# Kernel tuning notes

Measured on AMD Instinct MI355X. Metric: run time of the kernel, lower is better.

## Reference

```python
import jax, jax.numpy as jnp
import numpy as np

HDIM = 32
U_DIM = 8
HID = 128
T = 65536
DYN_GAIN = 0.02
STATE_DAMP = 0.1
H_CLIP = 5.0
DT = np.float32(5.0 / 60.0)  # 5 minutes in hours


def _xavier(key, shape):
    fan_in, fan_out = shape[0], shape[1]
    limit = np.sqrt(6.0 / (fan_in + fan_out)).astype(np.float32)
    return jax.random.uniform(key, shape, jnp.float32, -limit, limit)


def setup_inputs() -> dict:
    key = jax.random.key(0)
    ks = jax.random.split(key, 8)
    U = jax.random.normal(ks[0], (T, U_DIM), jnp.float32)
    params = {
        "U": U,
        "h0": jnp.zeros((1, HDIM), jnp.float32),
        "W1": _xavier(ks[1], (HDIM + U_DIM, HID)), "b1": jnp.zeros((HID,), jnp.float32),
        "W2": _xavier(ks[2], (HID, HID)), "b2": jnp.zeros((HID,), jnp.float32),
        "W3": _xavier(ks[3], (HID, HDIM)), "b3": jnp.zeros((HDIM,), jnp.float32),
        "Wd": _xavier(ks[4], (HDIM, 1)), "bd": jnp.zeros((1,), jnp.float32),
        "Wt": _xavier(ks[5], (HDIM, 1)), "bt": jnp.zeros((1,), jnp.float32),
        "Wc": _xavier(ks[6], (HDIM, 1)), "bc": jnp.zeros((1,), jnp.float32),
    }
    return params


def reference(U, h0, W1, b1, W2, b2, W3, b3, Wd, bd, Wt, bt, Wc, bc):
    dt = jnp.float32(DT)

    def dyn(h, u):
        # h: [1, HDIM], u: [1, U_DIM]
        x = jnp.concatenate([h, u], axis=-1)
        z = jax.nn.silu(x @ W1 + b1)
        z = jax.nn.silu(z @ W2 + b2)
        drift = z @ W3 + b3
        return DYN_GAIN * drift - STATE_DAMP * h

    def step(h, u_t):
        u = u_t[None, :]  # [1, U_DIM]
        # readout of current state (before the RK4 step, as in the torch loop)
        d = (h @ Wd + bd)[..., 0]  # [1]
        t = (h @ Wt + bt)[..., 0]
        c = (h @ Wc + bc)[..., 0]
        k1 = dyn(h, u)
        k2 = dyn(h + 0.5 * dt * k1, u)
        k3 = dyn(h + 0.5 * dt * k2, u)
        k4 = dyn(h + dt * k3, u)
        h_next = h + dt / 6.0 * (k1 + 2.0 * k2 + 2.0 * k3 + k4)
        h_next = jnp.nan_to_num(h_next, nan=0.0, posinf=0.0, neginf=0.0)
        h_next = jnp.clip(jnp.tanh(h_next), -H_CLIP, H_CLIP)
        return h_next, (d, t, c)

    h_last, (ds, ts, cs) = jax.lax.scan(step, h0, U)
    # ds/ts/cs: [T, 1] -> [T]
    return ds.squeeze(-1), ts.squeeze(-1), cs.squeeze(-1), h_last
```

## Files before the change

kernel.cpp:

```cpp
#include <hip/hip_runtime.h>
#include <math.h>


constexpr int T_STEPS = 65536;
constexpr int HD  = 32;
constexpr int HID = 128;

typedef float v2f __attribute__((ext_vector_type(2)));

__device__ __forceinline__ v2f fma2(v2f a, v2f b, v2f c) {
    return __builtin_elementwise_fma(a, b, c);
}

__device__ __forceinline__ float silu_f(float a) {
    return a / (1.0f + __expf(-a));
}

__device__ __forceinline__ void wg_barrier() {
    asm volatile("s_waitcnt lgkmcnt(0)" ::: "memory");
    __builtin_amdgcn_s_barrier();
    asm volatile("" ::: "memory");
}

__global__ __launch_bounds__(128, 1)
void node_scan(const float* __restrict__ U,
               const float* __restrict__ h0,
               const float* __restrict__ W1, const float* __restrict__ b1,
               const float* __restrict__ W2, const float* __restrict__ b2,
               const float* __restrict__ W3, const float* __restrict__ b3,
               const float* __restrict__ Wd, const float* __restrict__ bd,
               const float* __restrict__ Wt, const float* __restrict__ bt,
               const float* __restrict__ Wc, const float* __restrict__ bc,
               float* __restrict__ out)
{
    const int tid = threadIdx.x;
    const int j   = tid;
    const int m   = tid & 31;
    const int seg = tid >> 5;
    const int wv  = tid >> 6;

    __shared__ __align__(16) float xbuf[HD];
    __shared__ __align__(16) float z1buf[HID];
    __shared__ __align__(16) float z2buf[HID];
    __shared__ __align__(16) float pb2[64];

    v2f w1p[20];
#pragma unroll
    for (int i = 0; i < 20; ++i) {
        w1p[i].x = W1[(2 * i) * HID + j];
        w1p[i].y = W1[(2 * i + 1) * HID + j];
    }
    const float b1r = b1[j];

    v2f w2p[64];
#pragma unroll
    for (int i = 0; i < 64; ++i) {
        w2p[i].x = W2[(2 * i) * HID + j];
        w2p[i].y = W2[(2 * i + 1) * HID + j];
    }
    const float b2r = b2[j];

    v2f w3p[16];
#pragma unroll
    for (int i = 0; i < 16; ++i) {
        w3p[i].x = W3[(seg * 32 + 2 * i) * HD + m];
        w3p[i].y = W3[(seg * 32 + 2 * i + 1) * HD + m];
    }
    const float b3r = b3[m];

    const float whr = (wv == 0) ? Wd[m] : Wt[m];
    const float wcr = Wc[m];
    const float bd0 = bd[0], bt0 = bt[0], bc0 = bc[0];

    float hm   = h0[m];
    float xm   = hm;
    float kacc = 0.0f;

    const float DT  = 5.0f / 60.0f;
    const float HDT = 0.5f * DT;
    const float W6  = DT / 6.0f;

    float4 ua = *(const float4*)(U);
    float4 ub = *(const float4*)(U + 4);

    xbuf[m] = xm;
    wg_barrier();

    for (int t = 0; t < T_STEPS; ++t) {
        const int tn = (t + 1 < T_STEPS) ? (t + 1) : t;
        const float4 na = *(const float4*)(U + tn * 8);
        const float4 nb = *(const float4*)(U + tn * 8 + 4);

        {
            float p  = hm * whr;
            float pc = hm * wcr;
            p += __shfl_xor(p, 16);  pc += __shfl_xor(pc, 16);
            p += __shfl_xor(p, 8);   pc += __shfl_xor(pc, 8);
            p += __shfl_xor(p, 4);   pc += __shfl_xor(pc, 4);
            p += __shfl_xor(p, 2);   pc += __shfl_xor(pc, 2);
            p += __shfl_xor(p, 1);   pc += __shfl_xor(pc, 1);
            if (tid == 0)  { out[t] = p + bd0; out[2 * T_STEPS + t] = pc + bc0; }
            if (tid == 64) { out[T_STEPS + t] = p + bt0; }
        }

        float upj;
        {
            v2f u0; u0.x = ua.x; u0.y = ua.y;
            v2f u1; u1.x = ua.z; u1.y = ua.w;
            v2f u2; u2.x = ub.x; u2.y = ub.y;
            v2f u3; u3.x = ub.z; u3.y = ub.w;
            v2f up = {b1r, 0.0f};
            up = fma2(u0, w1p[16], up);
            up = fma2(u1, w1p[17], up);
            up = fma2(u2, w1p[18], up);
            up = fma2(u3, w1p[19], up);
            upj = up.x + up.y;
        }

#pragma unroll
        for (int st = 0; st < 4; ++st) {
            v2f a0 = {upj, 0.0f}, a1 = {0.0f, 0.0f};
            const float4* xv = (const float4*)xbuf;
#pragma unroll
            for (int i4 = 0; i4 < 8; ++i4) {
                const float4 v = xv[i4];
                v2f lo; lo.x = v.x; lo.y = v.y;
                v2f hi; hi.x = v.z; hi.y = v.w;
                a0 = fma2(lo, w1p[2 * i4],     a0);
                a1 = fma2(hi, w1p[2 * i4 + 1], a1);
            }
            const v2f as = a0 + a1;
            z1buf[j] = silu_f(as.x + as.y);
            wg_barrier();

            v2f c0 = {b2r, 0.0f}, c1 = {0.0f, 0.0f};
            v2f c2 = {0.0f, 0.0f}, c3 = {0.0f, 0.0f};
            const float4* z1v = (const float4*)z1buf;
#pragma unroll
            for (int i4 = 0; i4 < 32; ++i4) {
                const float4 v = z1v[i4];
                v2f lo; lo.x = v.x; lo.y = v.y;
                v2f hi; hi.x = v.z; hi.y = v.w;
                if (i4 & 1) {
                    c2 = fma2(lo, w2p[2 * i4],     c2);
                    c3 = fma2(hi, w2p[2 * i4 + 1], c3);
                } else {
                    c0 = fma2(lo, w2p[2 * i4],     c0);
                    c1 = fma2(hi, w2p[2 * i4 + 1], c1);
                }
            }
            const v2f cs = (c0 + c1) + (c2 + c3);
            z2buf[j] = silu_f(cs.x + cs.y);
            __builtin_amdgcn_wave_barrier();

            v2f p0 = {0.0f, 0.0f}, p1 = {0.0f, 0.0f};
            const float4* z2v = (const float4*)(z2buf + seg * 32);
#pragma unroll
            for (int i4 = 0; i4 < 8; ++i4) {
                const float4 v = z2v[i4];
                v2f lo; lo.x = v.x; lo.y = v.y;
                v2f hi; hi.x = v.z; hi.y = v.w;
                p0 = fma2(lo, w3p[2 * i4],     p0);
                p1 = fma2(hi, w3p[2 * i4 + 1], p1);
            }
            const v2f ps = p0 + p1;
            float pr = ps.x + ps.y;
            pr += __shfl_xor(pr, 32);
            pb2[wv * 32 + m] = pr;
            wg_barrier();

            {
                const float drift = (pb2[m] + pb2[m + 32]) + b3r;
                const float k = 0.02f * drift - 0.1f * xm;
                if (st == 0)      { kacc = k;           xm = hm + HDT * k; }
                else if (st == 1) { kacc += 2.0f * k;   xm = hm + HDT * k; }
                else if (st == 2) { kacc += 2.0f * k;   xm = hm + DT  * k; }
                else {
                    kacc += k;
                    float hn = hm + W6 * kacc;
                    if (!isfinite(hn)) hn = 0.0f;
                    hn = tanhf(hn);
                    hn = fminf(fmaxf(hn, -5.0f), 5.0f);
                    hm = hn; xm = hn;
                }
                xbuf[m] = xm;
            }
            __builtin_amdgcn_wave_barrier();
        }
        ua = na; ub = nb;
    }

    if (tid < HD) out[3 * T_STEPS + tid] = hm;
}

extern "C" void kernel_launch(void* const* d_in, const int* in_sizes, int n_in,
                              void* d_out, int out_size, void* d_ws, size_t ws_size,
                              hipStream_t stream) {
    const float* U  = (const float*)d_in[0];
    const float* h0 = (const float*)d_in[1];
    const float* W1 = (const float*)d_in[2];
    const float* b1 = (const float*)d_in[3];
    const float* W2 = (const float*)d_in[4];
    const float* b2 = (const float*)d_in[5];
    const float* W3 = (const float*)d_in[6];
    const float* b3 = (const float*)d_in[7];
    const float* Wd = (const float*)d_in[8];
    const float* bd = (const float*)d_in[9];
    const float* Wt = (const float*)d_in[10];
    const float* bt = (const float*)d_in[11];
    const float* Wc = (const float*)d_in[12];
    const float* bc = (const float*)d_in[13];
    float* out = (float*)d_out;

    node_scan<<<1, 128, 0, stream>>>(U, h0, W1, b1, W2, b2, W3, b3,
                                     Wd, bd, Wt, bt, Wc, bc, out);
}
```

Before: 237.5 ms.

## Split layer-2 matvec by input half per wave and exchange partial sums

Each wave now computes partial layer-2 sums for all 128 outputs over only its own 64 z1 inputs. That lets the barrier after the z1 write become a wave-local barrier. Partial sums are then exchanged through shared memory behind one workgroup barrier, and both waves redundantly compute the full z2 vector. W3 and the pb2 layouts are re-indexed to match the new z2 ordering. The aim is to shorten the cross-wave wait on the serial per-step critical path, at the cost of extra LDS traffic and duplicated silu work.

```diff
diff --git a/kernel.cpp b/kernel.cpp
--- a/kernel.cpp
+++ b/kernel.cpp
@@ -35,13 +35,15 @@
 {
     const int tid = threadIdx.x;
     const int j   = tid;
+    const int l   = tid & 63;
     const int m   = tid & 31;
     const int seg = tid >> 5;
     const int wv  = tid >> 6;
 
     __shared__ __align__(16) float xbuf[HD];
     __shared__ __align__(16) float z1buf[HID];
-    __shared__ __align__(16) float z2buf[HID];
+    __shared__ __align__(16) float z2slot[HID];
+    __shared__ __align__(16) float pex[2 * HID];
     __shared__ __align__(16) float pb2[64];
 
     v2f w1p[20];
@@ -52,19 +54,22 @@
     }
     const float b1r = b1[j];
 
-    v2f w2p[64];
-#pragma unroll
-    for (int i = 0; i < 64; ++i) {
-        w2p[i].x = W2[(2 * i) * HID + j];
-        w2p[i].y = W2[(2 * i + 1) * HID + j];
-    }
-    const float b2r = b2[j];
+    v2f w2a[32], w2b[32];
+#pragma unroll
+    for (int kp = 0; kp < 32; ++kp) {
+        const int k = wv * 64 + 2 * kp;
+        w2a[kp].x = W2[k * HID + l];
+        w2a[kp].y = W2[(k + 1) * HID + l];
+        w2b[kp].x = W2[k * HID + l + 64];
+        w2b[kp].y = W2[(k + 1) * HID + l + 64];
+    }
+    const float b2a = b2[l], b2b = b2[l + 64];
 
     v2f w3p[16];
 #pragma unroll
     for (int i = 0; i < 16; ++i) {
-        w3p[i].x = W3[(seg * 32 + 2 * i) * HD + m];
-        w3p[i].y = W3[(seg * 32 + 2 * i + 1) * HD + m];
+        w3p[i].x = W3[(seg * 16 + i) * HD + m];
+        w3p[i].y = W3[(seg * 16 + i + 64) * HD + m];
     }
     const float b3r = b3[m];
 
@@ -131,30 +136,38 @@
             }
             const v2f as = a0 + a1;
             z1buf[j] = silu_f(as.x + as.y);
-            wg_barrier();
-
-            v2f c0 = {b2r, 0.0f}, c1 = {0.0f, 0.0f};
-            v2f c2 = {0.0f, 0.0f}, c3 = {0.0f, 0.0f};
-            const float4* z1v = (const float4*)z1buf;
-#pragma unroll
-            for (int i4 = 0; i4 < 32; ++i4) {
+            __builtin_amdgcn_wave_barrier();
+
+            v2f aA0 = {0.0f, 0.0f}, aA1 = {0.0f, 0.0f};
+            v2f aB0 = {0.0f, 0.0f}, aB1 = {0.0f, 0.0f};
+            const float4* z1v = (const float4*)(z1buf + wv * 64);
+#pragma unroll
+            for (int i4 = 0; i4 < 16; ++i4) {
                 const float4 v = z1v[i4];
                 v2f lo; lo.x = v.x; lo.y = v.y;
                 v2f hi; hi.x = v.z; hi.y = v.w;
-                if (i4 & 1) {
-                    c2 = fma2(lo, w2p[2 * i4],     c2);
-                    c3 = fma2(hi, w2p[2 * i4 + 1], c3);
-                } else {
-                    c0 = fma2(lo, w2p[2 * i4],     c0);
-                    c1 = fma2(hi, w2p[2 * i4 + 1], c1);
-                }
-            }
-            const v2f cs = (c0 + c1) + (c2 + c3);
-            z2buf[j] = silu_f(cs.x + cs.y);
+                aA0 = fma2(lo, w2a[2 * i4],     aA0);
+                aA1 = fma2(hi, w2a[2 * i4 + 1], aA1);
+                aB0 = fma2(lo, w2b[2 * i4],     aB0);
+                aB1 = fma2(hi, w2b[2 * i4 + 1], aB1);
+            }
+            const v2f sA = aA0 + aA1;
+            const v2f sB = aB0 + aB1;
+            float2 mine;
+            mine.x = sA.x + sA.y;
+            mine.y = sB.x + sB.y;
+            ((float2*)pex)[wv * 64 + l] = mine;
+            wg_barrier();
+
+            const float2 po = ((const float2*)pex)[(1 ^ wv) * 64 + l];
+            const float z2A = silu_f(mine.x + po.x + b2a);
+            const float z2B = silu_f(mine.y + po.y + b2b);
+            float2 zs; zs.x = z2A; zs.y = z2B;
+            ((float2*)z2slot)[l] = zs;
             __builtin_amdgcn_wave_barrier();
 
             v2f p0 = {0.0f, 0.0f}, p1 = {0.0f, 0.0f};
-            const float4* z2v = (const float4*)(z2buf + seg * 32);
+            const float4* z2v = (const float4*)(z2slot + seg * 32);
 #pragma unroll
             for (int i4 = 0; i4 < 8; ++i4) {
                 const float4 v = z2v[i4];
@@ -166,11 +179,12 @@
             const v2f ps = p0 + p1;
             float pr = ps.x + ps.y;
             pr += __shfl_xor(pr, 32);
-            pb2[wv * 32 + m] = pr;
+            pb2[2 * m + wv] = pr;
             wg_barrier();
 
             {
-                const float drift = (pb2[m] + pb2[m + 32]) + b3r;
+                const float2 pp = ((const float2*)pb2)[m];
+                const float drift = (pp.x + pp.y) + b3r;
                 const float k = 0.02f * drift - 0.1f * xm;
                 if (st == 0)      { kacc = k;           xm = hm + HDT * k; }
                 else if (st == 1) { kacc += 2.0f * k;   xm = hm + HDT * k; }
```

Result: no change. 235.9 ms (-0.7%).

## Split second MLP layer's reduction across four waves with partial-sum exchange

Applied to the files above, without the earlier changes.

The block grows from 128 to 256 threads. Layer 2's K dimension is split between wave pairs, so each thread runs half as many serial FMAs and holds half as many W2 registers. The two partial sums are combined through shared memory behind one workgroup barrier. Layer 1 is now computed redundantly by both wave pairs so each wave can read its own z1 slice after only a wave barrier, and the readouts are spread so each wave handles one output. The goal is a shorter per-step critical path in this latency-bound serial scan, at the cost of more waves taking part in barriers and some duplicated layer-1 work.

```diff
diff --git a/kernel.cpp b/kernel.cpp
--- a/kernel.cpp
+++ b/kernel.cpp
@@ -22,7 +22,7 @@
     asm volatile("" ::: "memory");
 }
 
-__global__ __launch_bounds__(128, 1)
+__global__ __launch_bounds__(256, 1)
 void node_scan(const float* __restrict__ U,
                const float* __restrict__ h0,
                const float* __restrict__ W1, const float* __restrict__ b1,
@@ -34,43 +34,49 @@
                float* __restrict__ out)
 {
     const int tid = threadIdx.x;
-    const int j   = tid;
+    const int lam = tid & 63;
+    const int w   = tid >> 6;
+    const int wk  = w & 1;
+    const int wo  = w >> 1;
+    const int j1  = lam + wk * 64;
+    const int o   = lam + wo * 64;
     const int m   = tid & 31;
-    const int seg = tid >> 5;
-    const int wv  = tid >> 6;
+    const int sub = (tid >> 5) & 1;
 
     __shared__ __align__(16) float xbuf[HD];
     __shared__ __align__(16) float z1buf[HID];
     __shared__ __align__(16) float z2buf[HID];
-    __shared__ __align__(16) float pb2[64];
+    __shared__ __align__(16) float pex[2 * HID];
+    __shared__ __align__(16) float pdrift[64];
 
     v2f w1p[20];
 #pragma unroll
     for (int i = 0; i < 20; ++i) {
-        w1p[i].x = W1[(2 * i) * HID + j];
-        w1p[i].y = W1[(2 * i + 1) * HID + j];
-    }
-    const float b1r = b1[j];
-
-    v2f w2p[64];
-#pragma unroll
-    for (int i = 0; i < 64; ++i) {
-        w2p[i].x = W2[(2 * i) * HID + j];
-        w2p[i].y = W2[(2 * i + 1) * HID + j];
-    }
-    const float b2r = b2[j];
+        w1p[i].x = W1[(2 * i) * HID + j1];
+        w1p[i].y = W1[(2 * i + 1) * HID + j1];
+    }
+    const float b1r = b1[j1];
+
+    v2f w2p[32];
+#pragma unroll
+    for (int kp = 0; kp < 32; ++kp) {
+        const int k = wk * 64 + 2 * kp;
+        w2p[kp].x = W2[k * HID + o];
+        w2p[kp].y = W2[(k + 1) * HID + o];
+    }
+    const float b2r = b2[o];
 
     v2f w3p[16];
 #pragma unroll
     for (int i = 0; i < 16; ++i) {
-        w3p[i].x = W3[(seg * 32 + 2 * i) * HD + m];
-        w3p[i].y = W3[(seg * 32 + 2 * i + 1) * HD + m];
+        const int u0 = wo * 64 + sub * 32 + 2 * i;
+        w3p[i].x = W3[u0 * HD + m];
+        w3p[i].y = W3[(u0 + 1) * HD + m];
     }
     const float b3r = b3[m];
 
-    const float whr = (wv == 0) ? Wd[m] : Wt[m];
-    const float wcr = Wc[m];
-    const float bd0 = bd[0], bt0 = bt[0], bc0 = bc[0];
+    const float whr = (w == 0) ? Wd[m] : (w == 1) ? Wt[m] : (w == 2) ? Wc[m] : 0.0f;
+    const float bh  = (w == 0) ? bd[0] : (w == 1) ? bt[0] : (w == 2) ? bc[0] : 0.0f;
 
     float hm   = h0[m];
     float xm   = hm;
@@ -92,15 +98,13 @@
         const float4 nb = *(const float4*)(U + tn * 8 + 4);
 
         {
-            float p  = hm * whr;
-            float pc = hm * wcr;
-            p += __shfl_xor(p, 16);  pc += __shfl_xor(pc, 16);
-            p += __shfl_xor(p, 8);   pc += __shfl_xor(pc, 8);
-            p += __shfl_xor(p, 4);   pc += __shfl_xor(pc, 4);
-            p += __shfl_xor(p, 2);   pc += __shfl_xor(pc, 2);
-            p += __shfl_xor(p, 1);   pc += __shfl_xor(pc, 1);
-            if (tid == 0)  { out[t] = p + bd0; out[2 * T_STEPS + t] = pc + bc0; }
-            if (tid == 64) { out[T_STEPS + t] = p + bt0; }
+            float p = hm * whr;
+            p += __shfl_xor(p, 16);
+            p += __shfl_xor(p, 8);
+            p += __shfl_xor(p, 4);
+            p += __shfl_xor(p, 2);
+            p += __shfl_xor(p, 1);
+            if (lam == 0 && w < 3) out[w * T_STEPS + t] = p + bh;
         }
 
         float upj;
@@ -130,31 +134,31 @@
                 a1 = fma2(hi, w1p[2 * i4 + 1], a1);
             }
             const v2f as = a0 + a1;
-            z1buf[j] = silu_f(as.x + as.y);
-            wg_barrier();
-
-            v2f c0 = {b2r, 0.0f}, c1 = {0.0f, 0.0f};
-            v2f c2 = {0.0f, 0.0f}, c3 = {0.0f, 0.0f};
-            const float4* z1v = (const float4*)z1buf;
-#pragma unroll
-            for (int i4 = 0; i4 < 32; ++i4) {
+            z1buf[j1] = silu_f(as.x + as.y);
+            __builtin_amdgcn_wave_barrier();
+
+            v2f c0 = {0.0f, 0.0f}, c1 = {0.0f, 0.0f};
+            const float4* z1v = (const float4*)(z1buf + wk * 64);
+#pragma unroll
+            for (int i4 = 0; i4 < 16; ++i4) {
                 const float4 v = z1v[i4];
                 v2f lo; lo.x = v.x; lo.y = v.y;
                 v2f hi; hi.x = v.z; hi.y = v.w;
-                if (i4 & 1) {
-                    c2 = fma2(lo, w2p[2 * i4],     c2);
-                    c3 = fma2(hi, w2p[2 * i4 + 1], c3);
-                } else {
-                    c0 = fma2(lo, w2p[2 * i4],     c0);
-                    c1 = fma2(hi, w2p[2 * i4 + 1], c1);
-                }
-            }
-            const v2f cs = (c0 + c1) + (c2 + c3);
-            z2buf[j] = silu_f(cs.x + cs.y);
+                c0 = fma2(lo, w2p[2 * i4],     c0);
+                c1 = fma2(hi, w2p[2 * i4 + 1], c1);
+            }
+            const v2f cs = c0 + c1;
+            const float mine = cs.x + cs.y;
+            pex[wk * HID + o] = mine;
+            wg_barrier();
+
+            const float po = pex[(1 ^ wk) * HID + o];
+            const float z2 = silu_f(mine + po + b2r);
+            z2buf[o] = z2;
             __builtin_amdgcn_wave_barrier();
 
             v2f p0 = {0.0f, 0.0f}, p1 = {0.0f, 0.0f};
-            const float4* z2v = (const float4*)(z2buf + seg * 32);
+            const float4* z2v = (const float4*)(z2buf + wo * 64 + sub * 32);
 #pragma unroll
             for (int i4 = 0; i4 < 8; ++i4) {
                 const float4 v = z2v[i4];
@@ -166,11 +170,11 @@
             const v2f ps = p0 + p1;
             float pr = ps.x + ps.y;
             pr += __shfl_xor(pr, 32);
-            pb2[wv * 32 + m] = pr;
+            pdrift[wo * 32 + m] = pr;
             wg_barrier();
 
             {
-                const float drift = (pb2[m] + pb2[m + 32]) + b3r;
+                const float drift = (pdrift[m] + pdrift[m + 32]) + b3r;
                 const float k = 0.02f * drift - 0.1f * xm;
                 if (st == 0)      { kacc = k;           xm = hm + HDT * k; }
                 else if (st == 1) { kacc += 2.0f * k;   xm = hm + HDT * k; }
@@ -212,6 +216,6 @@
     const float* bc = (const float*)d_in[13];
     float* out = (float*)d_out;
 
-    node_scan<<<1, 128, 0, stream>>>(U, h0, W1, b1, W2, b2, W3, b3,
+    node_scan<<<1, 256, 0, stream>>>(U, h0, W1, b1, W2, b2, W3, b3,
                                      Wd, bd, Wt, bt, Wc, bc, out);
 }
```

Result: faster. 221.9 ms (median of 2 runs) (-6.5%).
